# Performance work log

Hardware: AMD Instinct MI355X
Metric: run time of the kernel (lower is better)

Reference implementation:

```python
import jax, jax.numpy as jnp
import numpy as np
from itertools import combinations

NUM_AUG = 10
EPS = 0.01
GAM3 = 0.01
NUM_PAIRS = 500


def setup_inputs() -> dict:
    key = jax.random.key(0)
    m, p = 4000, 256
    kx, ky = jax.random.split(key)
    X = jax.random.normal(kx, (m, p), dtype=jnp.float32)
    y = jax.random.randint(ky, (m,), 0, 400, dtype=jnp.int64)
    num_imgs = m // NUM_AUG
    # deterministic stand-in for np.random.choice over all image pairs
    rng = np.random.default_rng(0)
    pair_combs = np.array(list(combinations(range(num_imgs), 2)))
    sample_idx = rng.choice(len(pair_combs), NUM_PAIRS)
    sample_pairs = jnp.asarray(pair_combs[sample_idx], dtype=jnp.int32)  # [500, 2]
    return {"X": X, "y": y, "sample_pairs": sample_pairs}


def _pair_logdets(X, sample_pairs):
    # X: [m, p] so W = X.T is [p, m]; diagonal Pi selects num_aug columns of W
    # per image, i.e. contiguous rows of X -> W Pi W^T == seg^T @ seg.
    m, p = X.shape
    aug = jnp.arange(NUM_AUG)
    cols_i = sample_pairs[:, 0:1] * NUM_AUG + aug          # [S, 10]
    cols_j = sample_pairs[:, 1:2] * NUM_AUG + aug          # [S, 10]
    cols_pair = jnp.concatenate([cols_i, cols_j], axis=1)  # [S, 20]
    I = jnp.eye(p, dtype=X.dtype)

    def ld(cols, tr_pi):
        seg = X[cols]                                      # [S, k, p]
        gram = jnp.einsum('skp,skq->spq', seg, seg)        # [S, p, p] = W Pi W^T
        scalar = p / ((tr_pi + 1e-8) * EPS)
        return jnp.linalg.slogdet(I + scalar * gram)[1]    # [S]

    ld_pair = ld(cols_pair, 2.0 * NUM_AUG)  # trace(Pi) = 20
    ld_i = ld(cols_i, 1.0 * NUM_AUG)        # trace(Pi_i) = 10
    ld_j = ld(cols_j, 1.0 * NUM_AUG)        # trace(Pi_j) = 10
    return ld_pair, ld_i, ld_j


def reference(X, y, sample_pairs):
    ld_pair, ld_i, ld_j = _pair_logdets(X, sample_pairs)
    compress_loss_empi_ortho = jnp.mean(ld_pair - 0.5 * ld_i - 0.5 * ld_j)
    discrimn_loss_empi = jnp.mean(ld_pair)            # loss_d / num_pairs
    compress_loss_empi = jnp.mean(ld_i + ld_j)        # loss_c / num_pairs (detached in torch)
    total_loss_empi = GAM3 * -compress_loss_empi_ortho
    return (total_loss_empi, discrimn_loss_empi, compress_loss_empi,
            compress_loss_empi_ortho)
```

## Files before the change

kernel.cpp:

```cpp
#include <hip/hip_runtime.h>
#include <math.h>

#define NUM_AUG 10
#define S_PAIRS 500
#define P 256

typedef __attribute__((ext_vector_type(8))) short bf16x8;
typedef __attribute__((ext_vector_type(16))) float f32x16;

#define C_PAIR ((float)(256.0 / ((20.0 + 1e-8) * 0.01)))
#define C_SING ((float)(256.0 / ((10.0 + 1e-8) * 0.01)))

__device__ __forceinline__ unsigned short f2bf(float f) {
  unsigned u = __float_as_uint(f);
  unsigned r = (u + 0x7fffu + ((u >> 16) & 1u)) >> 16;
  return (unsigned short)r;
}

__global__ __launch_bounds__(64) void pair_kernel(
    const float* __restrict__ X,
    const int* __restrict__ pairs,
    float* __restrict__ out2 ) {
  __shared__ uint4 Sb4[32 * 512 / 16];
  __shared__ float G[20][21];
  char* Sb = (char*)Sb4;

  const int s = blockIdx.x;
  const int lane = threadIdx.x;
  const int i0 = pairs[2 * s + 0] * NUM_AUG;
  const int j0 = pairs[2 * s + 1] * NUM_AUG;

#pragma unroll
  for (int r = 0; r < 20; ++r) {
    const int gr = (r < 10) ? (i0 + r) : (j0 + (r - 10));
    const float4 v = *((const float4*)(X + (size_t)gr * P) + lane);
    uint2 w;
    w.x = (unsigned)f2bf(v.x) | ((unsigned)f2bf(v.y) << 16);
    w.y = (unsigned)f2bf(v.z) | ((unsigned)f2bf(v.w) << 16);
    const int off = r * 512 + ((lane * 8) ^ ((r & 15) << 4));
    *(uint2*)(Sb + off) = w;
  }
  __syncthreads();

  const int row = lane & 31;
  const int kg = lane >> 5;
  f32x16 acc;
#pragma unroll
  for (int i = 0; i < 16; ++i) acc[i] = 0.f;
#pragma unroll
  for (int kk = 0; kk < 16; ++kk) {
    const int cb = kk * 32 + kg * 16;
    const bf16x8 f = *(const bf16x8*)(Sb + row * 512 + (cb ^ ((row & 15) << 4)));
    acc = __builtin_amdgcn_mfma_f32_32x32x16_bf16(f, f, acc, 0, 0, 0);
  }
#pragma unroll
  for (int rg = 0; rg < 16; ++rg) {
    const int grow = (rg & 3) + 8 * (rg >> 2) + 4 * kg;
    const int gcol = row;
    if (grow < 20 && gcol < 20) G[grow][gcol] = acc[rg];
  }
  __syncthreads();

  const int grp = (lane < 32) ? 0 : (lane < 48) ? 1 : 2;
  const int base = (grp == 0) ? 0 : (grp == 1) ? 32 : 48;
  const int li = lane - base;
  const int n = (grp == 0) ? 20 : 10;
  const float cf = (grp == 0) ? C_PAIR : C_SING;
  const int r0 = (grp == 2) ? 10 : 0;

  float a[20];
#pragma unroll
  for (int k = 0; k < 20; ++k) {
    float g = 0.f;
    if (li < n && k < n) g = G[r0 + li][r0 + k];
    a[k] = cf * g + ((li == k) ? 1.f : 0.f);
  }

  float ld_acc = 0.f;
#pragma unroll
  for (int j = 0; j < 20; ++j) {
    const float dj = __shfl(a[j], base + j, 64);
    const float Ljj = sqrtf(dj);
    const float inv = 1.0f / Ljj;
    const float Lij = a[j] * inv;
    if (li == j && j < n) ld_acc += logf(Ljj);
#pragma unroll
    for (int k = j + 1; k < 20; ++k) {
      const float ck = __shfl(Lij, base + k, 64);
      if (k < n && li >= k) a[k] = fmaf(-Lij, ck, a[k]);
    }
  }

  float vp = (lane < 32) ? ld_acc : 0.f;
  float vs = (lane >= 32) ? ld_acc : 0.f;
#pragma unroll
  for (int m = 1; m < 64; m <<= 1) {
    vp += __shfl_xor(vp, m, 64);
    vs += __shfl_xor(vs, m, 64);
  }
  if (lane == 0) {
    out2[2 * s + 0] = 2.f * vp;
    out2[2 * s + 1] = 2.f * vs;
  }
}

__global__ __launch_bounds__(256) void reduce_kernel(
    const float* __restrict__ out2, float* __restrict__ out) {
  __shared__ float sh[4][2];
  const int tid = threadIdx.x;
  float sp = 0.f, sij = 0.f;
  for (int s = tid; s < S_PAIRS; s += 256) {
    sp += out2[2 * s + 0];
    sij += out2[2 * s + 1];
  }
  for (int off = 32; off; off >>= 1) {
    sp += __shfl_down(sp, off);
    sij += __shfl_down(sij, off);
  }
  const int wave = tid >> 6, lane = tid & 63;
  if (lane == 0) { sh[wave][0] = sp; sh[wave][1] = sij; }
  __syncthreads();
  if (tid == 0) {
    float tp = 0.f, tij = 0.f;
    for (int w = 0; w < 4; ++w) { tp += sh[w][0]; tij += sh[w][1]; }
    const float mp = tp / (float)S_PAIRS;
    const float mij = tij / (float)S_PAIRS;
    const float ortho = mp - 0.5f * mij;
    out[0] = -0.01f * ortho;
    out[1] = mp;
    out[2] = mij;
    out[3] = ortho;
  }
}

extern "C" void kernel_launch(void* const* d_in, const int* in_sizes, int n_in,
                              void* d_out, int out_size, void* d_ws, size_t ws_size,
                              hipStream_t stream) {
  const float* X = (const float*)d_in[0];
  const int* pairs = (const int*)d_in[2];
  float* out = (float*)d_out;
  float* ws = (float*)d_ws;

  pair_kernel<<<S_PAIRS, 64, 0, stream>>>(X, pairs, ws);
  reduce_kernel<<<1, 256, 0, stream>>>(ws, out);
}
```

Measured before the change: 15.39 us.

## Fuse reduction into pair kernel via atomic last-block pattern, load MFMA fragments directly

Merges the separate reduction kernel into the pair kernel: each block publishes its partial sums and increments an atomic counter, and the last block to finish does the final reduction. MFMA fragments are now built directly from global loads with packed bf16 conversion, which drops the LDS staging and one barrier. The accumulation is split across two accumulators to break the MFMA dependency chain. This saves a kernel launch but adds a memset launch, atomics, and a serialized final reduction in a single block.

```diff
diff --git a/kernel.cpp b/kernel.cpp
--- a/kernel.cpp
+++ b/kernel.cpp
@@ -1,4 +1,5 @@
 #include <hip/hip_runtime.h>
+#include <hip/hip_bf16.h>
 #include <math.h>
 
 #define NUM_AUG 10
@@ -11,53 +12,55 @@
 #define C_PAIR ((float)(256.0 / ((20.0 + 1e-8) * 0.01)))
 #define C_SING ((float)(256.0 / ((10.0 + 1e-8) * 0.01)))
 
-__device__ __forceinline__ unsigned short f2bf(float f) {
-  unsigned u = __float_as_uint(f);
-  unsigned r = (u + 0x7fffu + ((u >> 16) & 1u)) >> 16;
-  return (unsigned short)r;
+union pack2f { float f[2]; unsigned long long u; };
+union frag_u { bf16x8 v; unsigned u[4]; };
+
+__device__ __forceinline__ unsigned pk2(float a, float b) {
+  __hip_bfloat162 h = __float22bfloat162_rn(make_float2(a, b));
+  return *reinterpret_cast<unsigned*>(&h);
 }
 
-__global__ __launch_bounds__(64) void pair_kernel(
+__global__ __launch_bounds__(64) void fused_kernel(
     const float* __restrict__ X,
     const int* __restrict__ pairs,
-    float* __restrict__ out2 ) {
-  __shared__ uint4 Sb4[32 * 512 / 16];
+    unsigned long long* __restrict__ partial,
+    unsigned* __restrict__ counter,
+    float* __restrict__ out) {
   __shared__ float G[20][21];
-  char* Sb = (char*)Sb4;
 
   const int s = blockIdx.x;
   const int lane = threadIdx.x;
   const int i0 = pairs[2 * s + 0] * NUM_AUG;
   const int j0 = pairs[2 * s + 1] * NUM_AUG;
 
-#pragma unroll
-  for (int r = 0; r < 20; ++r) {
-    const int gr = (r < 10) ? (i0 + r) : (j0 + (r - 10));
-    const float4 v = *((const float4*)(X + (size_t)gr * P) + lane);
-    uint2 w;
-    w.x = (unsigned)f2bf(v.x) | ((unsigned)f2bf(v.y) << 16);
-    w.y = (unsigned)f2bf(v.z) | ((unsigned)f2bf(v.w) << 16);
-    const int off = r * 512 + ((lane * 8) ^ ((r & 15) << 4));
-    *(uint2*)(Sb + off) = w;
-  }
-  __syncthreads();
-
   const int row = lane & 31;
   const int kg = lane >> 5;
-  f32x16 acc;
+  const int gr = (row < 10) ? (i0 + row) : (row < 20 ? (j0 + row - 10) : i0);
+  const float* rp = X + (size_t)gr * P + kg * 8;
+
+  f32x16 acc0, acc1;
 #pragma unroll
-  for (int i = 0; i < 16; ++i) acc[i] = 0.f;
+  for (int i = 0; i < 16; ++i) { acc0[i] = 0.f; acc1[i] = 0.f; }
+
 #pragma unroll
   for (int kk = 0; kk < 16; ++kk) {
-    const int cb = kk * 32 + kg * 16;
-    const bf16x8 f = *(const bf16x8*)(Sb + row * 512 + (cb ^ ((row & 15) << 4)));
-    acc = __builtin_amdgcn_mfma_f32_32x32x16_bf16(f, f, acc, 0, 0, 0);
+    const float4 v0 = *(const float4*)(rp + kk * 16);
+    const float4 v1 = *(const float4*)(rp + kk * 16 + 4);
+    frag_u f;
+    f.u[0] = pk2(v0.x, v0.y);
+    f.u[1] = pk2(v0.z, v0.w);
+    f.u[2] = pk2(v1.x, v1.y);
+    f.u[3] = pk2(v1.z, v1.w);
+    if (kk & 1)
+      acc1 = __builtin_amdgcn_mfma_f32_32x32x16_bf16(f.v, f.v, acc1, 0, 0, 0);
+    else
+      acc0 = __builtin_amdgcn_mfma_f32_32x32x16_bf16(f.v, f.v, acc0, 0, 0, 0);
   }
+
 #pragma unroll
   for (int rg = 0; rg < 16; ++rg) {
     const int grow = (rg & 3) + 8 * (rg >> 2) + 4 * kg;
-    const int gcol = row;
-    if (grow < 20 && gcol < 20) G[grow][gcol] = acc[rg];
+    if (grow < 20 && row < 20) G[grow][row] = acc0[rg] + acc1[rg];
   }
   __syncthreads();
 
@@ -98,38 +101,41 @@
     vp += __shfl_xor(vp, m, 64);
     vs += __shfl_xor(vs, m, 64);
   }
+
+  unsigned old = 0;
   if (lane == 0) {
-    out2[2 * s + 0] = 2.f * vp;
-    out2[2 * s + 1] = 2.f * vs;
+    pack2f p;
+    p.f[0] = 2.f * vp;
+    p.f[1] = 2.f * vs;
+    __hip_atomic_store(&partial[s], p.u, __ATOMIC_RELEASE, __HIP_MEMORY_SCOPE_AGENT);
+    old = __hip_atomic_fetch_add(counter, 1u, __ATOMIC_ACQ_REL, __HIP_MEMORY_SCOPE_AGENT);
   }
-}
+  old = __shfl(old, 0, 64);
 
-__global__ __launch_bounds__(256) void reduce_kernel(
-    const float* __restrict__ out2, float* __restrict__ out) {
-  __shared__ float sh[4][2];
-  const int tid = threadIdx.x;
-  float sp = 0.f, sij = 0.f;
-  for (int s = tid; s < S_PAIRS; s += 256) {
-    sp += out2[2 * s + 0];
-    sij += out2[2 * s + 1];
-  }
-  for (int off = 32; off; off >>= 1) {
-    sp += __shfl_down(sp, off);
-    sij += __shfl_down(sij, off);
-  }
-  const int wave = tid >> 6, lane = tid & 63;
-  if (lane == 0) { sh[wave][0] = sp; sh[wave][1] = sij; }
-  __syncthreads();
-  if (tid == 0) {
-    float tp = 0.f, tij = 0.f;
-    for (int w = 0; w < 4; ++w) { tp += sh[w][0]; tij += sh[w][1]; }
-    const float mp = tp / (float)S_PAIRS;
-    const float mij = tij / (float)S_PAIRS;
-    const float ortho = mp - 0.5f * mij;
-    out[0] = -0.01f * ortho;
-    out[1] = mp;
-    out[2] = mij;
-    out[3] = ortho;
+  if (old == S_PAIRS - 1) {
+    __threadfence();
+    float sp = 0.f, sij = 0.f;
+#pragma unroll
+    for (int t = lane; t < S_PAIRS; t += 64) {
+      pack2f p;
+      p.u = __hip_atomic_load(&partial[t], __ATOMIC_ACQUIRE, __HIP_MEMORY_SCOPE_AGENT);
+      sp += p.f[0];
+      sij += p.f[1];
+    }
+#pragma unroll
+    for (int m = 1; m < 64; m <<= 1) {
+      sp += __shfl_xor(sp, m, 64);
+      sij += __shfl_xor(sij, m, 64);
+    }
+    if (lane == 0) {
+      const float mp = sp / (float)S_PAIRS;
+      const float mij = sij / (float)S_PAIRS;
+      const float ortho = mp - 0.5f * mij;
+      out[0] = -0.01f * ortho;
+      out[1] = mp;
+      out[2] = mij;
+      out[3] = ortho;
+    }
   }
 }
 
@@ -139,8 +145,10 @@
   const float* X = (const float*)d_in[0];
   const int* pairs = (const int*)d_in[2];
   float* out = (float*)d_out;
-  float* ws = (float*)d_ws;
 
-  pair_kernel<<<S_PAIRS, 64, 0, stream>>>(X, pairs, ws);
-  reduce_kernel<<<1, 256, 0, stream>>>(ws, out);
+  unsigned long long* partial = (unsigned long long*)d_ws;
+  unsigned* counter = (unsigned*)((char*)d_ws + 4096);
+
+  hipMemsetAsync(counter, 0, sizeof(unsigned), stream);
+  fused_kernel<<<S_PAIRS, 64, 0, stream>>>(X, pairs, partial, counter, out);
 }
```

Measured after the change: 34.26 us. 123% more time.
